# Optimization experiments

Hardware: AMD Instinct MI355X
Metric: run time of the kernel (lower is better)

## Reference

```python
import jax, jax.numpy as jnp
import numpy as np

CAPACITY_FACTOR = 1.25

def setup_inputs() -> dict:
    key = jax.random.key(0)
    ks = jax.random.split(key, 6)
    B, S, D, H, E = 4, 2048, 1024, 2048, 8
    x = jax.random.normal(ks[0], (B, S, D), dtype=jnp.float32)
    Wg = jax.random.normal(ks[1], (D, E), dtype=jnp.float32) / np.float32(np.sqrt(D))
    bg = jnp.zeros((E,), dtype=jnp.float32)
    W1 = jax.random.normal(ks[2], (E, H, D), dtype=jnp.float32) / np.float32(np.sqrt(H))
    W2 = jax.random.normal(ks[3], (E, D, H), dtype=jnp.float32) / np.float32(np.sqrt(D))
    W3 = jax.random.normal(ks[4], (E, D, H), dtype=jnp.float32) / np.float32(np.sqrt(D))
    return {"x": x, "Wg": Wg, "bg": bg, "W1": W1, "W2": W2, "W3": W3, "deterministic": 1}


def reference(x, Wg, bg, W1, W2, W3, deterministic):
    # deterministic=True path: no gate noise, no dropout (rate=0 anyway).
    b, s, d = x.shape
    E = W1.shape[0]
    xt = x.reshape(-1, d)                      # [N, d]
    N = xt.shape[0]
    cap = int(N / E * CAPACITY_FACTOR)

    logits = xt @ Wg + bg                      # [N, E]
    eid = jnp.argmax(logits, axis=1)           # [N] assigned expert (top-1)
    onehot = jax.nn.one_hot(eid, E, dtype=xt.dtype)
    # 0-based arrival position of each token within its expert's queue
    pos = (jnp.sum(jnp.cumsum(onehot, axis=0) * onehot, axis=1)).astype(jnp.int32) - 1
    valid = pos < cap                          # capacity mask (pos >= 0 always)
    slot = jnp.where(valid, pos, cap)          # overflow tokens -> dummy slot `cap`

    # Dispatch: scatter tokens into [E, cap+1, d]; slots unique among valid tokens
    buf = jnp.zeros((E, cap + 1, d), dtype=xt.dtype).at[eid, slot].set(xt)
    binp = buf[:, :cap]                        # [E, cap, d] (dummy slot dropped)

    # Grouped SwiGLU FFN per expert
    h = jax.nn.silu(jnp.einsum('ecd,edh->ech', binp, W2)) * jnp.einsum('ecd,edh->ech', binp, W3)
    bout = jnp.einsum('ech,ehd->ecd', h, W1)   # [E, cap, d]

    # Combine: gather each token's expert output; overflow tokens read zero row
    bout = jnp.concatenate([bout, jnp.zeros((E, 1, d), dtype=bout.dtype)], axis=1)
    eout = bout[eid, slot]                     # [N, d]

    weights = jax.nn.softmax(logits, axis=-1)
    gate_w = jnp.take_along_axis(weights, eid[:, None], axis=1)  # [N, 1]
    out = (gate_w * eout).reshape(b, s, d)
    return out
```

## Files before the change

### kernel.cpp

```cpp
#include <hip/hip_runtime.h>

#define N_TOK 8192
#define D_DIM 1024
#define H_DIM 2048
#define E_NUM 8
#define CAP   1280

typedef __attribute__((ext_vector_type(8))) short bf16x8;
typedef __attribute__((ext_vector_type(4))) float f32x4;

__device__ inline unsigned short f2bf(float f) {
  unsigned u = __float_as_uint(f);
  u += 0x7fffu + ((u >> 16) & 1u);
  return (unsigned short)(u >> 16);
}

#define VMCNT(n) asm volatile("s_waitcnt vmcnt(" #n ")" ::: "memory")
#define BARRIER() asm volatile("s_barrier" ::: "memory")

__device__ inline int xcd_chunked(int id, int na) {
  const int xcd = id & 7, pos = id >> 3;
  const int q = na >> 3, r = na & 7;
  return (xcd < r ? xcd * (q + 1) : r * (q + 1) + (xcd - r) * q) + pos;
}

__global__ __launch_bounds__(256) void transpose_cvt_all(const float* __restrict__ W2,
                                                         const float* __restrict__ W3,
                                                         const float* __restrict__ W1,
                                                         unsigned short* __restrict__ w2t,
                                                         unsigned short* __restrict__ w3t,
                                                         unsigned short* __restrict__ w1t) {
  __shared__ float tile[64][33];
  const int id = blockIdx.x;
  const float* src;
  unsigned short* dst;
  int R, C, bx, by, b;
  if (id < 16384) {
    const int q = id & 8191;
    b = q >> 10;
    const int rem = q & 1023;
    bx = rem & 63;
    by = rem >> 6;
    R = D_DIM; C = H_DIM;
    src = (id < 8192 ? W2 : W3);
    dst = (id < 8192 ? w2t : w3t);
  } else {
    const int q = id - 16384;
    b = q >> 10;
    const int rem = q & 1023;
    bx = rem & 31;
    by = rem >> 5;
    R = H_DIM; C = D_DIM;
    src = W1; dst = w1t;
  }
  src += (size_t)b * R * C;
  dst += (size_t)b * R * C;
  const int c0 = bx * 32, r0 = by * 64;
  const int tx = threadIdx.x & 31, ty = threadIdx.x >> 5;
#pragma unroll
  for (int i = 0; i < 8; ++i)
    tile[ty + i * 8][tx] = src[(size_t)(r0 + ty + i * 8) * C + c0 + tx];
  __syncthreads();
  const int rp = threadIdx.x & 31;
  const int cb = threadIdx.x >> 5;
#pragma unroll
  for (int it = 0; it < 4; ++it) {
    const int c = cb + it * 8;
    unsigned short v[2] = {f2bf(tile[2 * rp][c]), f2bf(tile[2 * rp + 1][c])};
    *reinterpret_cast<unsigned*>(dst + (size_t)(c0 + c) * R + r0 + 2 * rp) =
        *reinterpret_cast<unsigned*>(v);
  }
}

__global__ __launch_bounds__(256) void gate_kernel(const float* __restrict__ x,
                                                   const float* __restrict__ Wg,
                                                   const float* __restrict__ bg,
                                                   int* __restrict__ eid,
                                                   float* __restrict__ gatew) {
  __shared__ float wg[E_NUM][D_DIM];
  const int tid = threadIdx.x;
  for (int i = tid; i < D_DIM * E_NUM; i += 256) {
    int d = i >> 3, e = i & 7;
    wg[e][d] = Wg[i];
  }
  __syncthreads();
  const int w = tid >> 6, l = tid & 63;
  const int t = blockIdx.x * 4 + w;
  const float* xr = x + (size_t)t * D_DIM;
  float acc[8] = {0, 0, 0, 0, 0, 0, 0, 0};
#pragma unroll
  for (int i = 0; i < D_DIM / 64; ++i) {
    float xv = xr[l + 64 * i];
#pragma unroll
    for (int e = 0; e < 8; ++e) acc[e] += xv * wg[e][l + 64 * i];
  }
#pragma unroll
  for (int off = 32; off >= 1; off >>= 1) {
#pragma unroll
    for (int e = 0; e < 8; ++e) acc[e] += __shfl_xor(acc[e], off);
  }
  if (l == 0) {
    float best = -1e30f;
    int bi = 0;
#pragma unroll
    for (int e = 0; e < 8; ++e) {
      acc[e] += bg[e];
      if (acc[e] > best) { best = acc[e]; bi = e; }
    }
    float s = 0.f;
#pragma unroll
    for (int e = 0; e < 8; ++e) s += __expf(acc[e] - best);
    eid[t] = bi;
    gatew[t] = 1.f / s;
  }
}

__global__ __launch_bounds__(512) void scan_kernel(const int* __restrict__ eid,
                                                   int* __restrict__ slot,
                                                   int* __restrict__ tok_of,
                                                   int* __restrict__ work,
                                                   int* __restrict__ nwork) {
  __shared__ int se[N_TOK];
  __shared__ int nby[E_NUM];
  const int tid = threadIdx.x;
  for (int i = tid; i < N_TOK; i += 512) se[i] = eid[i];
  for (int i = tid; i < E_NUM * CAP; i += 512) tok_of[i] = -1;
  __syncthreads();
  const int e = tid >> 6;
  const int l = tid & 63;
  const unsigned long long lower = (l == 0) ? 0ull : ((1ull << l) - 1ull);
  int cnt = 0;
  for (int base = 0; base < N_TOK; base += 64) {
    const int t = base + l;
    const bool m = (se[t] == e);
    const unsigned long long bal = __ballot(m);
    if (m) {
      const int rank = cnt + __popcll(bal & lower);
      slot[t] = rank < CAP ? rank : CAP;
      if (rank < CAP) tok_of[e * CAP + rank] = t;
    }
    cnt += __popcll(bal);
  }
  if (l == 0) {
    const int c = cnt > CAP ? CAP : cnt;
    nby[e] = (c + 127) >> 7;
  }
  __syncthreads();
  if (tid == 0) {
    int n = 0;
    for (int ee = 0; ee < E_NUM; ++ee)
      for (int b = 0; b < nby[ee]; ++b) work[n++] = (ee << 4) | b;
    nwork[0] = n;
  }
}

#define SCAT_BLKS (E_NUM * CAP / 4)
__global__ __launch_bounds__(256) void scatter_zero_kernel(const float* __restrict__ x,
                                                           const int* __restrict__ tok_of,
                                                           const int* __restrict__ slot,
                                                           unsigned short* __restrict__ binp,
                                                           float* __restrict__ out) {
  const int l = threadIdx.x & 63;
  if (blockIdx.x < SCAT_BLKS) {
    const int row = blockIdx.x * 4 + (threadIdx.x >> 6);
    const int t = tok_of[row];
    unsigned short* dst = binp + (size_t)row * D_DIM;
    if (t >= 0) {
      const float* src = x + (size_t)t * D_DIM;
#pragma unroll
      for (int i = 0; i < 4; ++i) {
        const int d = (i * 64 + l) * 4;
        float4 v = *reinterpret_cast<const float4*>(src + d);
        unsigned short r[4] = {f2bf(v.x), f2bf(v.y), f2bf(v.z), f2bf(v.w)};
        *reinterpret_cast<uint2*>(dst + d) = *reinterpret_cast<uint2*>(r);
      }
    } else {
      uint2 z = {0u, 0u};
#pragma unroll
      for (int i = 0; i < 4; ++i) {
        const int d = (i * 64 + l) * 4;
        *reinterpret_cast<uint2*>(dst + d) = z;
      }
    }
  } else {
    const int t = (blockIdx.x - SCAT_BLKS) * 4 + (threadIdx.x >> 6);
    if (slot[t] < CAP) return;
    float4 z = {0.f, 0.f, 0.f, 0.f};
#pragma unroll
    for (int i = 0; i < 4; ++i)
      *reinterpret_cast<float4*>(out + (size_t)t * D_DIM + (i * 64 + l) * 4) = z;
  }
}

#define TILE64 (128 * 64)

__device__ inline void stage_tile(const unsigned short* __restrict__ g, int ldg, int k0,
                                  unsigned short* lds, int w, int l) {
  const int gcol = (l & 7) ^ (l >> 3);
  const unsigned short* gsrc = g + (size_t)(w * 32 + (l >> 3)) * ldg + k0 + gcol * 8;
#pragma unroll
  for (int it = 0; it < 4; ++it) {
    __builtin_amdgcn_global_load_lds(
        (const __attribute__((address_space(1))) unsigned int*)(gsrc + (size_t)(it * 8) * ldg),
        (__attribute__((address_space(3))) unsigned int*)(lds + (w * 32 + it * 8) * 64),
        16, 0, 0);
  }
}

__device__ inline bf16x8 lds_frag(const unsigned short* lds, int row, int c16) {
  return *reinterpret_cast<const bf16x8*>(lds + row * 64 + (c16 ^ (row & 7)) * 8);
}

__global__ __launch_bounds__(256, 2) void ffn1_kernel(const unsigned short* __restrict__ binp,
                                                      const unsigned short* __restrict__ w2t,
                                                      const unsigned short* __restrict__ w3t,
                                                      const int* __restrict__ work,
                                                      const int* __restrict__ nwork,
                                                      unsigned short* __restrict__ hbuf) {
  __shared__ unsigned short sA[TILE64], sB2[2][TILE64], sB3[2][TILE64];
  const int na = nwork[0] << 4;
  const int id = blockIdx.x;
  if (id >= na) return;
  const int wg = xcd_chunked(id, na);
  const int item = work[wg >> 4];
  const int e = item >> 4;
  const int by = item & 15;
  const int bx = wg & 15;
  const unsigned short* A  = binp + (size_t)e * CAP * D_DIM + (size_t)by * 128 * D_DIM;
  const unsigned short* B2 = w2t + (size_t)e * H_DIM * D_DIM + (size_t)bx * 128 * D_DIM;
  const unsigned short* B3 = w3t + (size_t)e * H_DIM * D_DIM + (size_t)bx * 128 * D_DIM;
  unsigned short* H = hbuf + (size_t)e * CAP * H_DIM;
  const int tid = threadIdx.x;
  const int l = tid & 63;
  const int w = tid >> 6, wr = w >> 1, wc = w & 1;
  f32x4 acc2[4][4] = {};
  f32x4 acc3[4][4] = {};

  stage_tile(B2, D_DIM, 0, sB2[0], w, l);
  stage_tile(B3, D_DIM, 0, sB3[0], w, l);

  const int NT = D_DIM / 64;
  int cur = 0;
  for (int kt = 0; kt < NT; ++kt) {
    stage_tile(A, D_DIM, kt * 64, sA, w, l);
    if (kt + 1 < NT) {
      stage_tile(B2, D_DIM, (kt + 1) * 64, sB2[cur ^ 1], w, l);
      stage_tile(B3, D_DIM, (kt + 1) * 64, sB3[cur ^ 1], w, l);
      VMCNT(8);
    } else {
      VMCNT(0);
    }
    BARRIER();
#pragma unroll
    for (int kk = 0; kk < 2; ++kk) {
      const int c16 = kk * 4 + (l >> 4);
      bf16x8 af[4], b2f[4], b3f[4];
#pragma unroll
      for (int f = 0; f < 4; ++f) {
        af[f]  = lds_frag(sA, wr * 64 + f * 16 + (l & 15), c16);
        b2f[f] = lds_frag(sB2[cur], wc * 64 + f * 16 + (l & 15), c16);
        b3f[f] = lds_frag(sB3[cur], wc * 64 + f * 16 + (l & 15), c16);
      }
#pragma unroll
      for (int fm = 0; fm < 4; ++fm)
#pragma unroll
        for (int fn = 0; fn < 4; ++fn) {
          acc2[fm][fn] = __builtin_amdgcn_mfma_f32_16x16x32_bf16(af[fm], b2f[fn], acc2[fm][fn], 0, 0, 0);
          acc3[fm][fn] = __builtin_amdgcn_mfma_f32_16x16x32_bf16(af[fm], b3f[fn], acc3[fm][fn], 0, 0, 0);
        }
    }
    BARRIER();
    cur ^= 1;
  }

  const int row0 = by * 128 + wr * 64;
  const int col0 = bx * 128 + wc * 64;
#pragma unroll
  for (int fm = 0; fm < 4; ++fm)
#pragma unroll
    for (int fn = 0; fn < 4; ++fn)
#pragma unroll
      for (int j = 0; j < 4; ++j) {
        const int row = row0 + fm * 16 + (l >> 4) * 4 + j;
        const int col = col0 + fn * 16 + (l & 15);
        const float v2 = acc2[fm][fn][j];
        const float v3 = acc3[fm][fn][j];
        const float hv = (v2 / (1.0f + __expf(-v2))) * v3;
        H[(size_t)row * H_DIM + col] = f2bf(hv);
      }
}

__global__ __launch_bounds__(256, 2) void ffn2_kernel(const unsigned short* __restrict__ hbuf,
                                                      const unsigned short* __restrict__ w1t,
                                                      const int* __restrict__ tok_of,
                                                      const float* __restrict__ gatew,
                                                      float* __restrict__ out) {
  __shared__ unsigned short sA[TILE64], sB[2][TILE64];
  const int id = (blockIdx.x & 7) * 80 + (blockIdx.x >> 3);
  const int e = id / 80;
  const int rem = id - e * 80;
  const int bx = rem / 10;
  const int by = rem - bx * 10;
  const int* tok = tok_of + e * CAP;
  if (tok[by * 128] < 0) return;
  const unsigned short* A = hbuf + (size_t)e * CAP * H_DIM + (size_t)by * 128 * H_DIM;
  const unsigned short* B = w1t + (size_t)e * D_DIM * H_DIM + (size_t)bx * 128 * H_DIM;
  const int tid = threadIdx.x;
  const int l = tid & 63;
  const int w = tid >> 6, wr = w >> 1, wc = w & 1;
  f32x4 acc[4][4] = {};

  stage_tile(B, H_DIM, 0, sB[0], w, l);

  const int NT = H_DIM / 64;
  int cur = 0;
  for (int kt = 0; kt < NT; ++kt) {
    stage_tile(A, H_DIM, kt * 64, sA, w, l);
    if (kt + 1 < NT) {
      stage_tile(B, H_DIM, (kt + 1) * 64, sB[cur ^ 1], w, l);
      VMCNT(4);
    } else {
      VMCNT(0);
    }
    BARRIER();
#pragma unroll
    for (int kk = 0; kk < 2; ++kk) {
      const int c16 = kk * 4 + (l >> 4);
      bf16x8 af[4], bfr[4];
#pragma unroll
      for (int f = 0; f < 4; ++f) {
        af[f]  = lds_frag(sA, wr * 64 + f * 16 + (l & 15), c16);
        bfr[f] = lds_frag(sB[cur], wc * 64 + f * 16 + (l & 15), c16);
      }
#pragma unroll
      for (int fm = 0; fm < 4; ++fm)
#pragma unroll
        for (int fn = 0; fn < 4; ++fn)
          acc[fm][fn] = __builtin_amdgcn_mfma_f32_16x16x32_bf16(af[fm], bfr[fn], acc[fm][fn], 0, 0, 0);
    }
    BARRIER();
    cur ^= 1;
  }

  const int row0 = by * 128 + wr * 64;
  const int col0 = bx * 128 + wc * 64;
#pragma unroll
  for (int fm = 0; fm < 4; ++fm)
#pragma unroll
    for (int j = 0; j < 4; ++j) {
      const int row = row0 + fm * 16 + (l >> 4) * 4 + j;
      const int t = tok[row];
      if (t >= 0) {
        const float g = gatew[t];
#pragma unroll
        for (int fn = 0; fn < 4; ++fn) {
          const int col = col0 + fn * 16 + (l & 15);
          out[(size_t)t * D_DIM + col] = g * acc[fm][fn][j];
        }
      }
    }
}

extern "C" void kernel_launch(void* const* d_in, const int* in_sizes, int n_in,
                              void* d_out, int out_size, void* d_ws, size_t ws_size,
                              hipStream_t stream) {
  const float* x  = (const float*)d_in[0];
  const float* Wg = (const float*)d_in[1];
  const float* bg = (const float*)d_in[2];
  const float* W1 = (const float*)d_in[3];
  const float* W2 = (const float*)d_in[4];
  const float* W3 = (const float*)d_in[5];
  float* out = (float*)d_out;

  char* ws = (char*)d_ws;
  unsigned short* w2t = (unsigned short*)ws; ws += (size_t)E_NUM * H_DIM * D_DIM * 2;
  unsigned short* w3t = (unsigned short*)ws; ws += (size_t)E_NUM * H_DIM * D_DIM * 2;
  unsigned short* w1t = (unsigned short*)ws; ws += (size_t)E_NUM * D_DIM * H_DIM * 2;
  unsigned short* binp = (unsigned short*)ws; ws += (size_t)E_NUM * CAP * D_DIM * 2;
  unsigned short* hbuf = (unsigned short*)ws; ws += (size_t)E_NUM * CAP * H_DIM * 2;
  int* eid = (int*)ws;    ws += (size_t)N_TOK * 4;
  float* gw = (float*)ws; ws += (size_t)N_TOK * 4;
  int* slot = (int*)ws;   ws += (size_t)N_TOK * 4;
  int* tok_of = (int*)ws; ws += (size_t)E_NUM * CAP * 4;
  int* work = (int*)ws;   ws += 128 * 4;
  int* nwork = (int*)ws;  ws += 4;

  transpose_cvt_all<<<24576, 256, 0, stream>>>(W2, W3, W1, w2t, w3t, w1t);
  gate_kernel<<<N_TOK / 4, 256, 0, stream>>>(x, Wg, bg, eid, gw);
  scan_kernel<<<1, 512, 0, stream>>>(eid, slot, tok_of, work, nwork);
  scatter_zero_kernel<<<SCAT_BLKS + N_TOK / 4, 256, 0, stream>>>(x, tok_of, slot, binp, out);
  ffn1_kernel<<<1280, 256, 0, stream>>>(binp, w2t, w3t, work, nwork, hbuf);
  ffn2_kernel<<<640, 256, 0, stream>>>(hbuf, w1t, tok_of, gw, out);
}
```

Before: 227.6 us.

## Fuse weight transpose and gating into one launch with vectorized accesses

Merges the weight transpose/bf16-convert kernel and the gate kernel into a single launch, with block ranges picking the role. The transpose now loads tiles with float4 reads and writes 8 bf16 values per thread in one 16-byte store. The gate path drops the LDS staging of Wg and reads it directly with float4 loads. This removes one launch and the gate's LDS fill, and widens the memory transactions of the weight conversion. The transpose's LDS tile is now also allocated for gate blocks.

New measurement: 233.5 us. +2.6%, slower.

```diff
diff --git a/kernel.cpp b/kernel.cpp
--- a/kernel.cpp
+++ b/kernel.cpp
@@ -24,94 +24,96 @@
   return (xcd < r ? xcd * (q + 1) : r * (q + 1) + (xcd - r) * q) + pos;
 }
 
-__global__ __launch_bounds__(256) void transpose_cvt_all(const float* __restrict__ W2,
-                                                         const float* __restrict__ W3,
-                                                         const float* __restrict__ W1,
-                                                         unsigned short* __restrict__ w2t,
-                                                         unsigned short* __restrict__ w3t,
-                                                         unsigned short* __restrict__ w1t) {
-  __shared__ float tile[64][33];
-  const int id = blockIdx.x;
-  const float* src;
-  unsigned short* dst;
-  int R, C, bx, by, b;
-  if (id < 16384) {
-    const int q = id & 8191;
-    b = q >> 10;
-    const int rem = q & 1023;
-    bx = rem & 63;
-    by = rem >> 6;
-    R = D_DIM; C = H_DIM;
-    src = (id < 8192 ? W2 : W3);
-    dst = (id < 8192 ? w2t : w3t);
-  } else {
-    const int q = id - 16384;
-    b = q >> 10;
-    const int rem = q & 1023;
-    bx = rem & 31;
-    by = rem >> 5;
-    R = H_DIM; C = D_DIM;
-    src = W1; dst = w1t;
-  }
-  src += (size_t)b * R * C;
-  dst += (size_t)b * R * C;
-  const int c0 = bx * 32, r0 = by * 64;
-  const int tx = threadIdx.x & 31, ty = threadIdx.x >> 5;
-#pragma unroll
-  for (int i = 0; i < 8; ++i)
-    tile[ty + i * 8][tx] = src[(size_t)(r0 + ty + i * 8) * C + c0 + tx];
-  __syncthreads();
-  const int rp = threadIdx.x & 31;
-  const int cb = threadIdx.x >> 5;
-#pragma unroll
-  for (int it = 0; it < 4; ++it) {
-    const int c = cb + it * 8;
-    unsigned short v[2] = {f2bf(tile[2 * rp][c]), f2bf(tile[2 * rp + 1][c])};
-    *reinterpret_cast<unsigned*>(dst + (size_t)(c0 + c) * R + r0 + 2 * rp) =
-        *reinterpret_cast<unsigned*>(v);
-  }
-}
-
-__global__ __launch_bounds__(256) void gate_kernel(const float* __restrict__ x,
+#define TR_BLKS 24576
+__global__ __launch_bounds__(256) void prep_kernel(const float* __restrict__ W2,
+                                                   const float* __restrict__ W3,
+                                                   const float* __restrict__ W1,
+                                                   unsigned short* __restrict__ w2t,
+                                                   unsigned short* __restrict__ w3t,
+                                                   unsigned short* __restrict__ w1t,
+                                                   const float* __restrict__ x,
                                                    const float* __restrict__ Wg,
                                                    const float* __restrict__ bg,
                                                    int* __restrict__ eid,
                                                    float* __restrict__ gatew) {
-  __shared__ float wg[E_NUM][D_DIM];
+  __shared__ float tile[64][33];
+  const int id = blockIdx.x;
   const int tid = threadIdx.x;
-  for (int i = tid; i < D_DIM * E_NUM; i += 256) {
-    int d = i >> 3, e = i & 7;
-    wg[e][d] = Wg[i];
-  }
-  __syncthreads();
-  const int w = tid >> 6, l = tid & 63;
-  const int t = blockIdx.x * 4 + w;
-  const float* xr = x + (size_t)t * D_DIM;
-  float acc[8] = {0, 0, 0, 0, 0, 0, 0, 0};
-#pragma unroll
-  for (int i = 0; i < D_DIM / 64; ++i) {
-    float xv = xr[l + 64 * i];
-#pragma unroll
-    for (int e = 0; e < 8; ++e) acc[e] += xv * wg[e][l + 64 * i];
-  }
-#pragma unroll
-  for (int off = 32; off >= 1; off >>= 1) {
-#pragma unroll
-    for (int e = 0; e < 8; ++e) acc[e] += __shfl_xor(acc[e], off);
-  }
-  if (l == 0) {
-    float best = -1e30f;
-    int bi = 0;
-#pragma unroll
-    for (int e = 0; e < 8; ++e) {
-      acc[e] += bg[e];
-      if (acc[e] > best) { best = acc[e]; bi = e; }
-    }
-    float s = 0.f;
-#pragma unroll
-    for (int e = 0; e < 8; ++e) s += __expf(acc[e] - best);
-    eid[t] = bi;
-    gatew[t] = 1.f / s;
+  if (id < TR_BLKS) {
+    const float* src;
+    unsigned short* dst;
+    int R, C, bx, by, b;
+    if (id < 16384) {
+      const int q = id & 8191;
+      b = q >> 10;
+      const int rem = q & 1023;
+      bx = rem & 63;
+      by = rem >> 6;
+      R = D_DIM; C = H_DIM;
+      src = (id < 8192 ? W2 : W3);
+      dst = (id < 8192 ? w2t : w3t);
+    } else {
+      const int q = id - 16384;
+      b = q >> 10;
+      const int rem = q & 1023;
+      bx = rem & 31;
+      by = rem >> 5;
+      R = H_DIM; C = D_DIM;
+      src = W1; dst = w1t;
+    }
+    src += (size_t)b * R * C;
+    dst += (size_t)b * R * C;
+    const int c0 = bx * 32, r0 = by * 64;
+    const int lrow = tid >> 3, lc4 = (tid & 7) * 4;
+#pragma unroll
+    for (int p = 0; p < 2; ++p) {
+      const float4 v = *reinterpret_cast<const float4*>(
+          src + (size_t)(r0 + lrow + p * 32) * C + c0 + lc4);
+      tile[lrow + p * 32][lc4 + 0] = v.x;
+      tile[lrow + p * 32][lc4 + 1] = v.y;
+      tile[lrow + p * 32][lc4 + 2] = v.z;
+      tile[lrow + p * 32][lc4 + 3] = v.w;
+    }
+    __syncthreads();
+    const int c = tid & 31, rg = tid >> 5;
+    unsigned short v8[8];
+#pragma unroll
+    for (int j = 0; j < 8; ++j) v8[j] = f2bf(tile[rg * 8 + j][c]);
+    *reinterpret_cast<bf16x8*>(dst + (size_t)(c0 + c) * R + r0 + rg * 8) =
+        *reinterpret_cast<const bf16x8*>(v8);
+  } else {
+    const int w = tid >> 6, l = tid & 63;
+    const int t = (id - TR_BLKS) * 4 + w;
+    const float* xr = x + (size_t)t * D_DIM;
+    float acc[8] = {0, 0, 0, 0, 0, 0, 0, 0};
+#pragma unroll
+    for (int i = 0; i < D_DIM / 64; ++i) {
+      const int d = l + 64 * i;
+      const float xv = xr[d];
+      const float4 w0 = *reinterpret_cast<const float4*>(Wg + (size_t)d * 8);
+      const float4 w1 = *reinterpret_cast<const float4*>(Wg + (size_t)d * 8 + 4);
+      acc[0] += xv * w0.x; acc[1] += xv * w0.y; acc[2] += xv * w0.z; acc[3] += xv * w0.w;
+      acc[4] += xv * w1.x; acc[5] += xv * w1.y; acc[6] += xv * w1.z; acc[7] += xv * w1.w;
+    }
+#pragma unroll
+    for (int off = 32; off >= 1; off >>= 1) {
+#pragma unroll
+      for (int e = 0; e < 8; ++e) acc[e] += __shfl_xor(acc[e], off);
+    }
+    if (l == 0) {
+      float best = -1e30f;
+      int bi = 0;
+#pragma unroll
+      for (int e = 0; e < 8; ++e) {
+        acc[e] += bg[e];
+        if (acc[e] > best) { best = acc[e]; bi = e; }
+      }
+      float s = 0.f;
+#pragma unroll
+      for (int e = 0; e < 8; ++e) s += __expf(acc[e] - best);
+      eid[t] = bi;
+      gatew[t] = 1.f / s;
+    }
   }
 }
 
@@ -385,8 +387,8 @@
   int* work = (int*)ws;   ws += 128 * 4;
   int* nwork = (int*)ws;  ws += 4;
 
-  transpose_cvt_all<<<24576, 256, 0, stream>>>(W2, W3, W1, w2t, w3t, w1t);
-  gate_kernel<<<N_TOK / 4, 256, 0, stream>>>(x, Wg, bg, eid, gw);
+  prep_kernel<<<TR_BLKS + N_TOK / 4, 256, 0, stream>>>(W2, W3, W1, w2t, w3t, w1t,
+                                                       x, Wg, bg, eid, gw);
   scan_kernel<<<1, 512, 0, stream>>>(eid, slot, tok_of, work, nwork);
   scatter_zero_kernel<<<SCAT_BLKS + N_TOK / 4, 256, 0, stream>>>(x, tok_of, slot, binp, out);
   ffn1_kernel<<<1280, 256, 0, stream>>>(binp, w2t, w3t, work, nwork, hbuf);
```
